# Performance work log

Hardware: AMD Instinct MI355X
Metric: run time of the kernel (lower is better)

Reference implementation:

```python
import jax, jax.numpy as jnp
import numpy as np


def _next_pow2(n: int) -> int:
    return 1 << (int(n) - 1).bit_length()


def setup_inputs() -> dict:
    key = jax.random.key(0)
    k1, k2 = jax.random.split(key)
    B, T, L = 256, 65536, 65536  # batch, seq_len, filter length (L >= T so epoched recurrence == full causal conv)
    x = jax.random.normal(k1, (B, T), dtype=jnp.float32)
    filt = jax.random.normal(k2, (1, L), dtype=jnp.float32) / np.float32(np.sqrt(L))
    return {"x": x, "filt": filt}


def reference(x, filt):
    """EpochedFutureFill.forward == causal FIR convolution of x with filt.

    The torch module's per-token loop (sliced dot-product + FFT-refreshed
    FutureFill cache every K steps) computes exactly
        y[:, t] = sum_{s=0}^{t} filt[0, s] * x[:, t - s]
    for t < T <= L. We express that directly as one FFT convolution,
    mirroring the module's own future_fill (pow-2 rfft/irfft) math.
    """
    B, T = x.shape
    L = filt.shape[-1]
    n_fft = _next_pow2(T + L - 1)
    xf = jnp.fft.rfft(x, n=n_fft)        # (B, n_fft//2+1) complex
    ff = jnp.fft.rfft(filt, n=n_fft)     # (1, n_fft//2+1) complex, broadcasts over batch
    y_full = jnp.fft.irfft(xf * ff, n=n_fft)
    return y_full[:, :T]                 # causal part: (B, T)
```

## Files before the change

### kernel.cpp

```cpp
#include <hip/hip_runtime.h>


#define N_FFT 131072
#define N1    512
#define N2    256
#define T_LEN 65536
#define CB    128
#define PI_F  3.14159265358979323846f
#define R2_F  0.70710678118654752f

typedef __attribute__((ext_vector_type(2))) __fp16 h2;
typedef __attribute__((ext_vector_type(4))) __fp16 h4;
typedef __attribute__((ext_vector_type(8))) __fp16 h8;

__device__ inline int brev9(int x) { return (int)(__brev((unsigned)x) >> 23); }

__device__ inline float2 cadd(float2 a, float2 b){ return make_float2(a.x+b.x, a.y+b.y); }
__device__ inline float2 csub(float2 a, float2 b){ return make_float2(a.x-b.x, a.y-b.y); }
__device__ inline float2 cmul(float2 a, float2 b){ return make_float2(a.x*b.x-a.y*b.y, a.x*b.y+a.y*b.x); }
__device__ inline float2 csq(float2 a){ return make_float2(a.x*a.x-a.y*a.y, 2.f*a.x*a.y); }
__device__ inline float2 conjf(float2 a){ return make_float2(a.x, -a.y); }
__device__ inline float2 expif(float a){ float s,c; __sincosf(a,&s,&c); return make_float2(c,s); }
__device__ inline h2 f2h(float2 v){ return __builtin_amdgcn_cvt_pkrtz(v.x, v.y); }
__device__ inline float2 mul_ipow(float2 a, int g){
    float2 b = (g & 1) ? make_float2(-a.y, a.x) : a;
    return (g & 2) ? make_float2(-b.x, -b.y) : b;
}

__device__ inline void dif4(float2&a0, float2&a1, float2&a2, float2&a3, float2 w1, float2 w2){
    float2 s02 = cadd(a0,a2), d02 = csub(a0,a2);
    float2 s13 = cadd(a1,a3), d13 = csub(a1,a3);
    float2 b2 = cmul(w1,d02);
    float2 t  = cmul(w1,d13);
    float2 b3 = make_float2(t.y, -t.x);
    a0 = cadd(s02,s13);
    a1 = cmul(w2, csub(s02,s13));
    a2 = cadd(b2,b3);
    a3 = cmul(w2, csub(b2,b3));
}

__device__ inline void dit4i(float2&a0, float2&a1, float2&a2, float2&a3, float2 w1, float2 w2){
    float2 t1 = cmul(w1,a1), t3 = cmul(w1,a3);
    float2 u0 = cadd(a0,t1), u1 = csub(a0,t1);
    float2 u2 = cadd(a2,t3), u3 = csub(a2,t3);
    float2 s2 = cmul(w2,u2), s3 = cmul(w2,u3);
    a0 = cadd(u0,s2); a2 = csub(u0,s2);
    a1 = make_float2(u1.x - s3.y, u1.y + s3.x);
    a3 = make_float2(u1.x + s3.y, u1.y - s3.x);
}

template<bool HALF>
__global__ __launch_bounds__(512, 4) void fwd_cols(
    const float* __restrict__ re_base, const float* __restrict__ im_base,
    long long row_stride, void* __restrict__ dstv)
{
    __shared__ float2 s[N1 * 16];
    const int tile = blockIdx.x, row = blockIdx.y, tid = threadIdx.x;
    const int n2base = tile * 16;
    const float* rp = re_base + (long long)row * row_stride;
    const float* ip = im_base ? (im_base + (long long)row * row_stride) : nullptr;

    {
        const int cp = tid & 7, n1g = tid >> 3;
#pragma unroll
        for (int i = 0; i < 4; i++) {
            int n1 = n1g + 64 * i;
            int g  = n1 * N2 + n2base + 2 * cp;
            float2 a = *(const float2*)(rp + g);
            float2 b = ip ? *(const float2*)(ip + g) : make_float2(0.f, 0.f);
            s[n1 * 16 + 2 * cp]     = make_float2(a.x, b.x);
            s[n1 * 16 + 2 * cp + 1] = make_float2(a.y, b.y);
        }
    }
    __syncthreads();

    const int c = tid & 15, r = tid >> 4;

    {
        float2 w1 = expif((float)r * (-PI_F / 256.f));
        const float2 stp = make_float2(0.92387953251f, -0.38268343236f);
#pragma unroll
        for (int qq = 0; qq < 4; qq++) {
            int j = r + 32 * qq;
            float2 w2 = csq(w1);
            float2 a0 = s[j * 16 + c], a1 = s[(j + 128) * 16 + c];
            float2 b2 = cmul(w1, a0);
            float2 t  = cmul(w1, a1);
            float2 b3 = make_float2(t.y, -t.x);
            s[j * 16 + c]         = cadd(a0, a1);
            s[(j + 128) * 16 + c] = cmul(w2, csub(a0, a1));
            s[(j + 256) * 16 + c] = cadd(b2, b3);
            s[(j + 384) * 16 + c] = cmul(w2, csub(b2, b3));
            w1 = cmul(w1, stp);
        }
    }
    __syncthreads();

    {
        float2 w1 = expif((float)r * (-PI_F / 64.f));
        float2 w2 = csq(w1);
#pragma unroll
        for (int qq = 0; qq < 4; qq++) {
            int p0 = qq * 128 + r;
            float2 a0 = s[p0*16+c], a1 = s[(p0+32)*16+c], a2 = s[(p0+64)*16+c], a3 = s[(p0+96)*16+c];
            dif4(a0, a1, a2, a3, w1, w2);
            s[p0*16+c] = a0; s[(p0+32)*16+c] = a1; s[(p0+64)*16+c] = a2; s[(p0+96)*16+c] = a3;
        }
    }
    __syncthreads();

    {
        float2 w1 = expif((float)(r & 7) * (-PI_F / 16.f));
        float2 w2 = csq(w1);
#pragma unroll
        for (int qq = 0; qq < 4; qq++) {
            int g = (r >> 3) + 4 * qq;
            int p0 = g * 32 + (r & 7);
            float2 a0 = s[p0*16+c], a1 = s[(p0+8)*16+c], a2 = s[(p0+16)*16+c], a3 = s[(p0+24)*16+c];
            dif4(a0, a1, a2, a3, w1, w2);
            s[p0*16+c] = a0; s[(p0+8)*16+c] = a1; s[(p0+16)*16+c] = a2; s[(p0+24)*16+c] = a3;
        }
    }
    __syncthreads();

    const int n2 = n2base + c;
    const float2 w1c = make_float2(R2_F, -R2_F);
    const float2 w2c = make_float2(0.f, -1.f);
    const float2 one = make_float2(1.f, 0.f);
    const float2 w64 = expif((float)n2 * (-PI_F / 1024.f));
#pragma unroll
    for (int o = 0; o < 2; o++) {
        int base = 8 * (r + 32 * o);
        float2 v[8];
#pragma unroll
        for (int m = 0; m < 8; m++) v[m] = s[(base + m) * 16 + c];
        dif4(v[0], v[2], v[4], v[6], one, one);
        dif4(v[1], v[3], v[5], v[7], w1c, w2c);
#pragma unroll
        for (int m = 0; m < 8; m += 2) {
            float2 a = v[m], b = v[m + 1];
            v[m] = cadd(a, b); v[m + 1] = csub(a, b);
        }
        const int Kb = brev9(base);
        float2 wK = expif((float)(n2 * Kb) * (-2.f * PI_F / (float)N_FFT));
        float2 pw[8];
        pw[0] = one;
#pragma unroll
        for (int k = 1; k < 8; k++) pw[k] = cmul(pw[k-1], w64);
        const int b3tab[8] = {0,4,2,6,1,5,3,7};
#pragma unroll
        for (int m = 0; m < 8; m++) {
            int b  = b3tab[m];
            int k1 = Kb + 64 * b;
            float2 w = cmul(wK, pw[b]);
            float2 rv = cmul(v[m], w);
            if (HALF) {
                h2* drow = (h2*)dstv + (size_t)row * N_FFT;
                drow[(size_t)k1 * N2 + n2] = f2h(rv);
            } else {
                float2* drow = (float2*)dstv + (size_t)row * N_FFT;
                drow[(size_t)k1 * N2 + n2] = rv;
            }
        }
    }
}

#define MROW 288
#define MIDX(rw, p) ((rw) * MROW + (p) + 2 * ((p) >> 4))

__global__ __launch_bounds__(256) void fwd_rows_g(float2* __restrict__ G)
{
    __shared__ float2 s[8 * MROW];
    const int tid = threadIdx.x;
    const long long rbase = (long long)blockIdx.x * 8;
#pragma unroll
    for (int i = 0; i < 8; i++) {
        int e = tid + 256 * i, rw = e >> 8, p = e & 255;
        s[MIDX(rw, p)] = G[(rbase + rw) * N2 + p];
    }
    __syncthreads();
    const int rl = tid >> 5, rr = tid & 31;
#pragma unroll
    for (int qq = 0; qq < 2; qq++) {
        int j = rr + 32 * qq;
        float2 w1 = expif((float)j * (-PI_F / 128.f)), w2 = csq(w1);
        float2 a0=s[MIDX(rl,j)], a1=s[MIDX(rl,j+64)], a2=s[MIDX(rl,j+128)], a3=s[MIDX(rl,j+192)];
        dif4(a0,a1,a2,a3,w1,w2);
        s[MIDX(rl,j)]=a0; s[MIDX(rl,j+64)]=a1; s[MIDX(rl,j+128)]=a2; s[MIDX(rl,j+192)]=a3;
    }
    __syncthreads();
#pragma unroll
    for (int qq = 0; qq < 2; qq++) {
        int q = rr + 32 * qq, j = q & 15, g = q >> 4, p0 = g * 64 + j;
        float2 w1 = expif((float)j * (-PI_F / 32.f)), w2 = csq(w1);
        float2 a0=s[MIDX(rl,p0)], a1=s[MIDX(rl,p0+16)], a2=s[MIDX(rl,p0+32)], a3=s[MIDX(rl,p0+48)];
        dif4(a0,a1,a2,a3,w1,w2);
        s[MIDX(rl,p0)]=a0; s[MIDX(rl,p0+16)]=a1; s[MIDX(rl,p0+32)]=a2; s[MIDX(rl,p0+48)]=a3;
    }
    __syncthreads();
#pragma unroll
    for (int qq = 0; qq < 2; qq++) {
        int q = rr + 32 * qq, j = q & 3, g = q >> 2, p0 = g * 16 + j;
        float2 w1 = expif((float)j * (-PI_F / 8.f)), w2 = csq(w1);
        float2 a0=s[MIDX(rl,p0)], a1=s[MIDX(rl,p0+4)], a2=s[MIDX(rl,p0+8)], a3=s[MIDX(rl,p0+12)];
        dif4(a0,a1,a2,a3,w1,w2);
        s[MIDX(rl,p0)]=a0; s[MIDX(rl,p0+4)]=a1; s[MIDX(rl,p0+8)]=a2; s[MIDX(rl,p0+12)]=a3;
    }
    __syncthreads();
#pragma unroll
    for (int qq = 0; qq < 2; qq++) {
        int base = 4 * (rr + 32 * qq);
        float2 a0=s[MIDX(rl,base)], a1=s[MIDX(rl,base+1)], a2=s[MIDX(rl,base+2)], a3=s[MIDX(rl,base+3)];
        float2 s02 = cadd(a0,a2), d02 = csub(a0,a2);
        float2 s13 = cadd(a1,a3), d13 = csub(a1,a3);
        float2 b3 = make_float2(d13.y, -d13.x);
        s[MIDX(rl,base)]   = cadd(s02,s13);
        s[MIDX(rl,base+1)] = csub(s02,s13);
        s[MIDX(rl,base+2)] = cadd(d02,b3);
        s[MIDX(rl,base+3)] = csub(d02,b3);
    }
    __syncthreads();
#pragma unroll
    for (int i = 0; i < 8; i++) {
        int e = tid + 256 * i, rw = e >> 8, p = e & 255;
        G[(rbase + rw) * N2 + p] = s[MIDX(rw, p)];
    }
}

__global__ __launch_bounds__(512) void mid_rows(
    h2* __restrict__ buf, const float2* __restrict__ Gb)
{
    __shared__ float4 s4[(8 * MROW) / 2];
    float2* s = (float2*)s4;
    const int tid = threadIdx.x;
    const long long rbase = (long long)blockIdx.x * 8;

    const int rl = tid >> 6, rr = tid & 63;
    const int k1 = (int)((rbase + rl) & (N1 - 1));

    const int rB = rl * MROW;
    const int b1 = rB + rr + ((rr >> 4) << 1);
    const int b2 = rB + 72 * (rr >> 4) + (rr & 15);
    const int b3 = rB + 18 * (rr >> 2) + (rr & 3);
    const int si = 144 * rl + 2 * rr + (rr >> 2);

    const float2 u0 = expif((float)rr * (-PI_F / 128.f));
    const float2 u1 = csq(csq(u0));
    const float2 u2 = csq(csq(u1));
    const float2 f2 = mul_ipow(u1, rr >> 4);
    const float2 f3 = mul_ipow(u2, rr >> 2);

    {
        h8 v = *((const h8*)(buf + ((rbase + rl) * N2 + 4 * rr)));
        s4[si]     = make_float4((float)v[0], (float)v[1], (float)v[2], (float)v[3]);
        s4[si + 1] = make_float4((float)v[4], (float)v[5], (float)v[6], (float)v[7]);
    }
    __syncthreads();

    {
        float2 w2 = csq(u0);
        float2 a0=s[b1], a1=s[b1+72], a2=s[b1+144], a3=s[b1+216];
        dif4(a0,a1,a2,a3,u0,w2);
        s[b1]=a0; s[b1+72]=a1; s[b1+144]=a2; s[b1+216]=a3;
    }
    __syncthreads();
    {
        float2 w2 = csq(f2);
        float2 a0=s[b2], a1=s[b2+18], a2=s[b2+36], a3=s[b2+54];
        dif4(a0,a1,a2,a3,f2,w2);
        s[b2]=a0; s[b2+18]=a1; s[b2+36]=a2; s[b2+54]=a3;
    }
    __syncthreads();
    {
        float2 w2 = csq(f3);
        float2 a0=s[b3], a1=s[b3+4], a2=s[b3+8], a3=s[b3+12];
        dif4(a0,a1,a2,a3,f3,w2);
        s[b3]=a0; s[b3+4]=a1; s[b3+8]=a2; s[b3+12]=a3;
    }
    __syncthreads();

    {
        int base = 4 * rr;
        float4 q01 = s4[si], q23 = s4[si + 1];
        float2 a0 = make_float2(q01.x, q01.y), a1 = make_float2(q01.z, q01.w);
        float2 a2 = make_float2(q23.x, q23.y), a3 = make_float2(q23.z, q23.w);
        float2 s02 = cadd(a0,a2), d02 = csub(a0,a2);
        float2 s13 = cadd(a1,a3), d13 = csub(a1,a3);
        float2 b3v = make_float2(d13.y, -d13.x);
        float2 v0 = cadd(s02,s13), v1 = csub(s02,s13), v2 = cadd(d02,b3v), v3 = csub(d02,b3v);
        const float4* g4 = (const float4*)(Gb + (size_t)k1 * N2);
        float4 g01 = g4[base >> 1], g23 = g4[(base >> 1) + 1];
        v0 = cmul(v0, make_float2(g01.x, g01.y));
        v1 = cmul(v1, make_float2(g01.z, g01.w));
        v2 = cmul(v2, make_float2(g23.x, g23.y));
        v3 = cmul(v3, make_float2(g23.z, g23.w));
        float2 u0v = cadd(v0,v1), u1v = csub(v0,v1);
        float2 u2v = cadd(v2,v3), u3v = csub(v2,v3);
        float2 r0 = cadd(u0v,u2v), r2 = csub(u0v,u2v);
        float2 r1 = make_float2(u1v.x - u3v.y, u1v.y + u3v.x);
        float2 r3 = make_float2(u1v.x + u3v.y, u1v.y - u3v.x);
        s4[si]     = make_float4(r0.x, r0.y, r1.x, r1.y);
        s4[si + 1] = make_float4(r2.x, r2.y, r3.x, r3.y);
    }
    __syncthreads();

    {
        float2 w2 = conjf(f3), w1 = csq(w2);
        float2 a0=s[b3], a1=s[b3+4], a2=s[b3+8], a3=s[b3+12];
        dit4i(a0,a1,a2,a3,w1,w2);
        s[b3]=a0; s[b3+4]=a1; s[b3+8]=a2; s[b3+12]=a3;
    }
    __syncthreads();
    {
        float2 w2 = conjf(f2), w1 = csq(w2);
        float2 a0=s[b2], a1=s[b2+18], a2=s[b2+36], a3=s[b2+54];
        dit4i(a0,a1,a2,a3,w1,w2);
        s[b2]=a0; s[b2+18]=a1; s[b2+36]=a2; s[b2+54]=a3;
    }
    __syncthreads();
    {
        float2 w2 = conjf(u0), w1 = csq(w2);
        float2 a0=s[b1], a1=s[b1+72], a2=s[b1+144], a3=s[b1+216];
        dit4i(a0,a1,a2,a3,w1,w2);
        s[b1]=a0; s[b1+72]=a1; s[b1+144]=a2; s[b1+216]=a3;
    }
    __syncthreads();

    {
        const int pp0 = 4 * rr;
        const float th = 2.f * PI_F / (float)N_FFT;
        float2 w = expif((float)(pp0 * k1) * th);
        float2 stp = expif((float)k1 * th);
        float4 q01 = s4[si], q23 = s4[si + 1];
        float2 r0 = cmul(make_float2(q01.x, q01.y), w); w = cmul(w, stp);
        float2 r1 = cmul(make_float2(q01.z, q01.w), w); w = cmul(w, stp);
        float2 r2 = cmul(make_float2(q23.x, q23.y), w); w = cmul(w, stp);
        float2 r3 = cmul(make_float2(q23.z, q23.w), w);
        union { h8 v8; h2 v2[4]; } U;
        U.v2[0] = f2h(r0); U.v2[1] = f2h(r1); U.v2[2] = f2h(r2); U.v2[3] = f2h(r3);
        *((h8*)(buf + ((rbase + rl) * N2 + pp0))) = U.v8;
    }
}

__global__ __launch_bounds__(512, 4) void inv_cols(
    const h2* __restrict__ src, float* __restrict__ out)
{
    __shared__ float4 s4[N1 * 16 / 2];
    float2* s = (float2*)s4;
    const int tile = blockIdx.x, row = blockIdx.y, tid = threadIdx.x;
    const int n2base = tile * 16;
    const h2* srow = src + (size_t)row * N_FFT;
    const int cp = tid & 7, r8 = tid >> 3;

#pragma unroll
    for (int i = 0; i < 8; i++) {
        int k1 = r8 + 64 * i;
        h4 v = *((const h4*)(srow + (size_t)k1 * N2 + n2base + 2 * cp));
        int p = brev9(k1);
        s4[p * 8 + cp] = make_float4((float)v.x, (float)v.y, (float)v.z, (float)v.w);
    }
    __syncthreads();

    const int c = tid & 15, r = tid >> 4;

    const float2 w1c = make_float2(0.f, 1.f);
    const float2 w2c = make_float2(R2_F, R2_F);
    const float2 one = make_float2(1.f, 0.f);
#pragma unroll
    for (int o = 0; o < 2; o++) {
        int base = 8 * (r + 32 * o);
        float2 v[8];
#pragma unroll
        for (int m = 0; m < 8; m++) v[m] = s[(base + m) * 16 + c];
#pragma unroll
        for (int m = 0; m < 8; m += 2) {
            float2 a = v[m], b = v[m + 1];
            v[m] = cadd(a, b); v[m + 1] = csub(a, b);
        }
        dit4i(v[0], v[2], v[4], v[6], one, one);
        dit4i(v[1], v[3], v[5], v[7], w1c, w2c);
#pragma unroll
        for (int m = 0; m < 8; m++) s[(base + m) * 16 + c] = v[m];
    }
    __syncthreads();

    {
        float2 w2 = expif((float)(r & 7) * (PI_F / 16.f));
        float2 w1 = csq(w2);
#pragma unroll
        for (int qq = 0; qq < 4; qq++) {
            int g = (r >> 3) + 4 * qq;
            int p0 = g * 32 + (r & 7);
            float2 a0 = s[p0*16+c], a1 = s[(p0+8)*16+c], a2 = s[(p0+16)*16+c], a3 = s[(p0+24)*16+c];
            dit4i(a0, a1, a2, a3, w1, w2);
            s[p0*16+c] = a0; s[(p0+8)*16+c] = a1; s[(p0+16)*16+c] = a2; s[(p0+24)*16+c] = a3;
        }
    }
    __syncthreads();
    {
        float2 w2 = expif((float)r * (PI_F / 64.f));
        float2 w1 = csq(w2);
#pragma unroll
        for (int qq = 0; qq < 4; qq++) {
            int p0 = qq * 128 + r;
            float2 a0 = s[p0*16+c], a1 = s[(p0+32)*16+c], a2 = s[(p0+64)*16+c], a3 = s[(p0+96)*16+c];
            dit4i(a0, a1, a2, a3, w1, w2);
            s[p0*16+c] = a0; s[(p0+32)*16+c] = a1; s[(p0+64)*16+c] = a2; s[(p0+96)*16+c] = a3;
        }
    }
    __syncthreads();
    {
        float2 w2 = expif((float)r * (PI_F / 256.f));
        const float2 stp = make_float2(0.92387953251f, 0.38268343236f);
#pragma unroll
        for (int qq = 0; qq < 4; qq++) {
            int j = r + 32 * qq;
            float2 w1 = csq(w2);
            float2 a0 = s[j*16+c], a1 = s[(j+128)*16+c], a2 = s[(j+256)*16+c], a3 = s[(j+384)*16+c];
            dit4i(a0, a1, a2, a3, w1, w2);
            s[j*16+c] = a0; s[(j+128)*16+c] = a1; s[(j+256)*16+c] = a2; s[(j+384)*16+c] = a3;
            w2 = cmul(w2, stp);
        }
    }
    __syncthreads();

    const float scale = 1.0f / (float)N_FFT;
    float* out0 = out + (size_t)(2 * row) * T_LEN;
    float* out1 = out + (size_t)(2 * row + 1) * T_LEN;
#pragma unroll
    for (int i = 0; i < 4; i++) {
        int p = r8 + 64 * i;
        float4 q = s4[p * 8 + cp];
        int n = p * N2 + n2base + 2 * cp;
        *(float2*)(out0 + n) = make_float2(q.x * scale, q.z * scale);
        *(float2*)(out1 + n) = make_float2(q.y * scale, q.w * scale);
    }
}

extern "C" void kernel_launch(void* const* d_in, const int* in_sizes, int n_in,
                              void* d_out, int out_size, void* d_ws, size_t ws_size,
                              hipStream_t stream) {
    const float* x    = (const float*)d_in[0];
    const float* filt = (const float*)d_in[1];
    float* out = (float*)d_out;

    h2* buf = (h2*)d_ws;
    float2* G = (float2*)((char*)d_ws + (size_t)CB * N_FFT * sizeof(h2));

    fwd_cols<false><<<dim3(16, 1), 512, 0, stream>>>(filt, nullptr, 0LL, (void*)G);
    fwd_rows_g<<<N1 / 8, 256, 0, stream>>>(G);
    fwd_cols<true><<<dim3(16, CB), 512, 0, stream>>>(x, x + T_LEN, (long long)(2 * T_LEN), (void*)buf);
    mid_rows<<<(CB * N1) / 8, 512, 0, stream>>>(buf, G);
    inv_cols<<<dim3(16, CB), 512, 0, stream>>>(buf, out);
}
```

Before: 232.4 us.

## Rewrite 256-point row FFTs as register-resident 16x16 decomposition

Replaces the radix-4 shared-memory passes in fwd_rows_g and mid_rows, which needed several barriers, with a 16x16 four-step FFT. Each thread holds 16 points in registers and does two fft16 passes with one LDS transpose, using a shared twiddle table. Each 16-lane row group syncs only with an lgkmcnt wait, and mid_rows now handles 16 rows per 256-thread block. This cuts LDS traffic, barriers and per-thread sincos work. The cost is more registers per thread and narrower h2 global loads and stores with a 16-element stride.

```diff
diff --git a/kernel.cpp b/kernel.cpp
--- a/kernel.cpp
+++ b/kernel.cpp
@@ -8,6 +8,8 @@
 #define CB    128
 #define PI_F  3.14159265358979323846f
 #define R2_F  0.70710678118654752f
+#define C16F  0.92387953251128675613f
+#define S16F  0.38268343236508977173f
 
 typedef __attribute__((ext_vector_type(2))) __fp16 h2;
 typedef __attribute__((ext_vector_type(4))) __fp16 h4;
@@ -18,14 +20,18 @@
 __device__ inline float2 cadd(float2 a, float2 b){ return make_float2(a.x+b.x, a.y+b.y); }
 __device__ inline float2 csub(float2 a, float2 b){ return make_float2(a.x-b.x, a.y-b.y); }
 __device__ inline float2 cmul(float2 a, float2 b){ return make_float2(a.x*b.x-a.y*b.y, a.x*b.y+a.y*b.x); }
+__device__ inline float2 cmulc(float2 a, float2 b){ return make_float2(a.x*b.x+a.y*b.y, a.y*b.x-a.x*b.y); }
 __device__ inline float2 csq(float2 a){ return make_float2(a.x*a.x-a.y*a.y, 2.f*a.x*a.y); }
 __device__ inline float2 conjf(float2 a){ return make_float2(a.x, -a.y); }
 __device__ inline float2 expif(float a){ float s,c; __sincosf(a,&s,&c); return make_float2(c,s); }
 __device__ inline h2 f2h(float2 v){ return __builtin_amdgcn_cvt_pkrtz(v.x, v.y); }
-__device__ inline float2 mul_ipow(float2 a, int g){
-    float2 b = (g & 1) ? make_float2(-a.y, a.x) : a;
-    return (g & 2) ? make_float2(-b.x, -b.y) : b;
-}
+
+__device__ inline float2 mul_mi(float2 a){ return make_float2(a.y, -a.x); }
+__device__ inline float2 mul_pi(float2 a){ return make_float2(-a.y, a.x); }
+__device__ inline float2 mul_w81(float2 a){ return make_float2(R2_F*(a.x+a.y), R2_F*(a.y-a.x)); }
+__device__ inline float2 mul_w83(float2 a){ return make_float2(R2_F*(a.y-a.x), -R2_F*(a.x+a.y)); }
+__device__ inline float2 mul_w81c(float2 a){ return make_float2(R2_F*(a.x-a.y), R2_F*(a.x+a.y)); }
+__device__ inline float2 mul_w83c(float2 a){ return make_float2(-R2_F*(a.x+a.y), R2_F*(a.x-a.y)); }
 
 __device__ inline void dif4(float2&a0, float2&a1, float2&a2, float2&a3, float2 w1, float2 w2){
     float2 s02 = cadd(a0,a2), d02 = csub(a0,a2);
@@ -47,6 +53,99 @@
     a0 = cadd(u0,s2); a2 = csub(u0,s2);
     a1 = make_float2(u1.x - s3.y, u1.y + s3.x);
     a3 = make_float2(u1.x + s3.y, u1.y - s3.x);
+}
+
+__device__ constexpr int BR[16] = {0,8,4,12,2,10,6,14,1,9,5,13,3,11,7,15};
+
+__device__ __forceinline__ void fft16_fwd(float2 v[16]){
+    {
+        float2 s02=cadd(v[0],v[8]),  d02=csub(v[0],v[8]);
+        float2 s13=cadd(v[4],v[12]), d13=csub(v[4],v[12]);
+        float2 b3 = mul_mi(d13);
+        v[0]=cadd(s02,s13); v[4]=csub(s02,s13);
+        v[8]=cadd(d02,b3);  v[12]=csub(d02,b3);
+    }
+    {
+        float2 s02=cadd(v[1],v[9]),  d02=csub(v[1],v[9]);
+        float2 s13=cadd(v[5],v[13]), d13=csub(v[5],v[13]);
+        const float2 w1 = make_float2(C16F,-S16F);
+        float2 b2 = cmul(w1,d02), b3 = mul_mi(cmul(w1,d13));
+        v[1]=cadd(s02,s13);  v[5]=mul_w81(csub(s02,s13));
+        v[9]=cadd(b2,b3);    v[13]=mul_w81(csub(b2,b3));
+    }
+    {
+        float2 s02=cadd(v[2],v[10]), d02=csub(v[2],v[10]);
+        float2 s13=cadd(v[6],v[14]), d13=csub(v[6],v[14]);
+        float2 b2 = mul_w81(d02), b3 = mul_mi(mul_w81(d13));
+        v[2]=cadd(s02,s13);  v[6]=mul_mi(csub(s02,s13));
+        v[10]=cadd(b2,b3);   v[14]=mul_mi(csub(b2,b3));
+    }
+    {
+        float2 s02=cadd(v[3],v[11]), d02=csub(v[3],v[11]);
+        float2 s13=cadd(v[7],v[15]), d13=csub(v[7],v[15]);
+        const float2 w1 = make_float2(S16F,-C16F);
+        float2 b2 = cmul(w1,d02), b3 = mul_mi(cmul(w1,d13));
+        v[3]=cadd(s02,s13);  v[7]=mul_w83(csub(s02,s13));
+        v[11]=cadd(b2,b3);   v[15]=mul_w83(csub(b2,b3));
+    }
+#pragma unroll
+    for (int q=0;q<4;q++){
+        float2 a0=v[4*q],a1=v[4*q+1],a2=v[4*q+2],a3=v[4*q+3];
+        float2 s02=cadd(a0,a2), d02=csub(a0,a2);
+        float2 s13=cadd(a1,a3), d13=csub(a1,a3);
+        float2 b3 = mul_mi(d13);
+        v[4*q]=cadd(s02,s13);   v[4*q+1]=csub(s02,s13);
+        v[4*q+2]=cadd(d02,b3);  v[4*q+3]=csub(d02,b3);
+    }
+}
+
+__device__ __forceinline__ void fft16_inv(float2 v[16]){
+#pragma unroll
+    for (int q=0;q<4;q++){
+        float2 a0=v[4*q],a1=v[4*q+1],a2=v[4*q+2],a3=v[4*q+3];
+        float2 u0=cadd(a0,a1), u1=csub(a0,a1);
+        float2 u2=cadd(a2,a3), u3=csub(a2,a3);
+        v[4*q]=cadd(u0,u2);   v[4*q+2]=csub(u0,u2);
+        v[4*q+1]=make_float2(u1.x-u3.y, u1.y+u3.x);
+        v[4*q+3]=make_float2(u1.x+u3.y, u1.y-u3.x);
+    }
+    {
+        float2 t1=v[4], t3=v[12];
+        float2 u0=cadd(v[0],t1), u1=csub(v[0],t1);
+        float2 u2=cadd(v[8],t3), u3=csub(v[8],t3);
+        v[0]=cadd(u0,u2); v[8]=csub(u0,u2);
+        v[4]=make_float2(u1.x-u3.y, u1.y+u3.x);
+        v[12]=make_float2(u1.x+u3.y, u1.y-u3.x);
+    }
+    {
+        float2 t1=mul_w81c(v[5]), t3=mul_w81c(v[13]);
+        float2 u0=cadd(v[1],t1), u1=csub(v[1],t1);
+        float2 u2=cadd(v[9],t3), u3=csub(v[9],t3);
+        const float2 w2 = make_float2(C16F,S16F);
+        float2 s2=cmul(w2,u2), s3=cmul(w2,u3);
+        v[1]=cadd(u0,s2); v[9]=csub(u0,s2);
+        v[5]=make_float2(u1.x-s3.y, u1.y+s3.x);
+        v[13]=make_float2(u1.x+s3.y, u1.y-s3.x);
+    }
+    {
+        float2 t1=mul_pi(v[6]), t3=mul_pi(v[14]);
+        float2 u0=cadd(v[2],t1), u1=csub(v[2],t1);
+        float2 u2=cadd(v[10],t3), u3=csub(v[10],t3);
+        float2 s2=mul_w81c(u2), s3=mul_w81c(u3);
+        v[2]=cadd(u0,s2); v[10]=csub(u0,s2);
+        v[6]=make_float2(u1.x-s3.y, u1.y+s3.x);
+        v[14]=make_float2(u1.x+s3.y, u1.y-s3.x);
+    }
+    {
+        float2 t1=mul_w83c(v[7]), t3=mul_w83c(v[15]);
+        float2 u0=cadd(v[3],t1), u1=csub(v[3],t1);
+        float2 u2=cadd(v[11],t3), u3=csub(v[11],t3);
+        const float2 w2 = make_float2(S16F,C16F);
+        float2 s2=cmul(w2,u2), s3=cmul(w2,u3);
+        v[3]=cadd(u0,s2); v[11]=csub(u0,s2);
+        v[7]=make_float2(u1.x-s3.y, u1.y+s3.x);
+        v[15]=make_float2(u1.x+s3.y, u1.y-s3.x);
+    }
 }
 
 template<bool HALF>
@@ -165,180 +264,128 @@
     }
 }
 
-#define MROW 288
-#define MIDX(rw, p) ((rw) * MROW + (p) + 2 * ((p) >> 4))
-
-__global__ __launch_bounds__(256) void fwd_rows_g(float2* __restrict__ G)
+#define RPITCH 18
+
+__global__ __launch_bounds__(128) void fwd_rows_g(float2* __restrict__ G)
 {
-    __shared__ float2 s[8 * MROW];
+    __shared__ __align__(16) float2 s[8 * 16 * RPITCH + 16 * RPITCH];
     const int tid = threadIdx.x;
-    const long long rbase = (long long)blockIdx.x * 8;
-#pragma unroll
-    for (int i = 0; i < 8; i++) {
-        int e = tid + 256 * i, rw = e >> 8, p = e & 255;
-        s[MIDX(rw, p)] = G[(rbase + rw) * N2 + p];
-    }
-    __syncthreads();
-    const int rl = tid >> 5, rr = tid & 31;
-#pragma unroll
-    for (int qq = 0; qq < 2; qq++) {
-        int j = rr + 32 * qq;
-        float2 w1 = expif((float)j * (-PI_F / 128.f)), w2 = csq(w1);
-        float2 a0=s[MIDX(rl,j)], a1=s[MIDX(rl,j+64)], a2=s[MIDX(rl,j+128)], a3=s[MIDX(rl,j+192)];
-        dif4(a0,a1,a2,a3,w1,w2);
-        s[MIDX(rl,j)]=a0; s[MIDX(rl,j+64)]=a1; s[MIDX(rl,j+128)]=a2; s[MIDX(rl,j+192)]=a3;
-    }
-    __syncthreads();
-#pragma unroll
-    for (int qq = 0; qq < 2; qq++) {
-        int q = rr + 32 * qq, j = q & 15, g = q >> 4, p0 = g * 64 + j;
-        float2 w1 = expif((float)j * (-PI_F / 32.f)), w2 = csq(w1);
-        float2 a0=s[MIDX(rl,p0)], a1=s[MIDX(rl,p0+16)], a2=s[MIDX(rl,p0+32)], a3=s[MIDX(rl,p0+48)];
-        dif4(a0,a1,a2,a3,w1,w2);
-        s[MIDX(rl,p0)]=a0; s[MIDX(rl,p0+16)]=a1; s[MIDX(rl,p0+32)]=a2; s[MIDX(rl,p0+48)]=a3;
-    }
-    __syncthreads();
-#pragma unroll
-    for (int qq = 0; qq < 2; qq++) {
-        int q = rr + 32 * qq, j = q & 3, g = q >> 2, p0 = g * 16 + j;
-        float2 w1 = expif((float)j * (-PI_F / 8.f)), w2 = csq(w1);
-        float2 a0=s[MIDX(rl,p0)], a1=s[MIDX(rl,p0+4)], a2=s[MIDX(rl,p0+8)], a3=s[MIDX(rl,p0+12)];
-        dif4(a0,a1,a2,a3,w1,w2);
-        s[MIDX(rl,p0)]=a0; s[MIDX(rl,p0+4)]=a1; s[MIDX(rl,p0+8)]=a2; s[MIDX(rl,p0+12)]=a3;
-    }
-    __syncthreads();
-#pragma unroll
-    for (int qq = 0; qq < 2; qq++) {
-        int base = 4 * (rr + 32 * qq);
-        float2 a0=s[MIDX(rl,base)], a1=s[MIDX(rl,base+1)], a2=s[MIDX(rl,base+2)], a3=s[MIDX(rl,base+3)];
-        float2 s02 = cadd(a0,a2), d02 = csub(a0,a2);
-        float2 s13 = cadd(a1,a3), d13 = csub(a1,a3);
-        float2 b3 = make_float2(d13.y, -d13.x);
-        s[MIDX(rl,base)]   = cadd(s02,s13);
-        s[MIDX(rl,base+1)] = csub(s02,s13);
-        s[MIDX(rl,base+2)] = cadd(d02,b3);
-        s[MIDX(rl,base+3)] = csub(d02,b3);
-    }
-    __syncthreads();
-#pragma unroll
-    for (int i = 0; i < 8; i++) {
-        int e = tid + 256 * i, rw = e >> 8, p = e & 255;
-        G[(rbase + rw) * N2 + p] = s[MIDX(rw, p)];
-    }
-}
-
-__global__ __launch_bounds__(512) void mid_rows(
-    h2* __restrict__ buf, const float2* __restrict__ Gb)
+    const int t = tid & 15, rl = tid >> 4;
+    const long long row = (long long)blockIdx.x * 8 + rl;
+    float2* tab = s + 8 * 16 * RPITCH;
+
+    {
+        int b0 = tid >> 4, c0 = tid & 15;
+        tab[b0 * RPITCH + c0] = expif((float)(b0 * c0) * (-2.f * PI_F / 256.f));
+        int e = tid + 128, b1 = e >> 4, c1 = e & 15;
+        tab[b1 * RPITCH + c1] = expif((float)(b1 * c1) * (-2.f * PI_F / 256.f));
+    }
+    __syncthreads();
+
+    const float2* gp = G + (size_t)row * N2 + t;
+    float2 v[16];
+#pragma unroll
+    for (int a = 0; a < 16; a++) v[a] = gp[16 * a];
+
+    fft16_fwd(v);
+#pragma unroll
+    for (int p = 1; p < 16; p++) v[p] = cmul(v[p], tab[t * RPITCH + BR[p]]);
+
+    float2* rS = s + rl * (16 * RPITCH);
+    float4* rS4 = (float4*)rS;
+#pragma unroll
+    for (int k = 0; k < 8; k++) {
+        float2 e = v[BR[2*k]], o = v[BR[2*k] + 8];
+        rS4[(t * RPITCH + 2*k) >> 1] = make_float4(e.x, e.y, o.x, o.y);
+    }
+    asm volatile("s_waitcnt lgkmcnt(0)" ::: "memory");
+#pragma unroll
+    for (int b = 0; b < 16; b++) v[b] = rS[b * RPITCH + t];
+
+    fft16_fwd(v);
+
+    float4* o4 = (float4*)(G + (size_t)row * N2 + 16 * t);
+#pragma unroll
+    for (int m = 0; m < 8; m++)
+        o4[m] = make_float4(v[2*m].x, v[2*m].y, v[2*m+1].x, v[2*m+1].y);
+}
+
+__global__ __launch_bounds__(256, 4) void mid_rows(
+    h2* __restrict__ buf, const float2* __restrict__ Gh)
 {
-    __shared__ float4 s4[(8 * MROW) / 2];
-    float2* s = (float2*)s4;
+    __shared__ __align__(16) float2 s[16 * 16 * RPITCH + 16 * RPITCH];
     const int tid = threadIdx.x;
-    const long long rbase = (long long)blockIdx.x * 8;
-
-    const int rl = tid >> 6, rr = tid & 63;
-    const int k1 = (int)((rbase + rl) & (N1 - 1));
-
-    const int rB = rl * MROW;
-    const int b1 = rB + rr + ((rr >> 4) << 1);
-    const int b2 = rB + 72 * (rr >> 4) + (rr & 15);
-    const int b3 = rB + 18 * (rr >> 2) + (rr & 3);
-    const int si = 144 * rl + 2 * rr + (rr >> 2);
-
-    const float2 u0 = expif((float)rr * (-PI_F / 128.f));
-    const float2 u1 = csq(csq(u0));
-    const float2 u2 = csq(csq(u1));
-    const float2 f2 = mul_ipow(u1, rr >> 4);
-    const float2 f3 = mul_ipow(u2, rr >> 2);
-
-    {
-        h8 v = *((const h8*)(buf + ((rbase + rl) * N2 + 4 * rr)));
-        s4[si]     = make_float4((float)v[0], (float)v[1], (float)v[2], (float)v[3]);
-        s4[si + 1] = make_float4((float)v[4], (float)v[5], (float)v[6], (float)v[7]);
-    }
-    __syncthreads();
-
-    {
-        float2 w2 = csq(u0);
-        float2 a0=s[b1], a1=s[b1+72], a2=s[b1+144], a3=s[b1+216];
-        dif4(a0,a1,a2,a3,u0,w2);
-        s[b1]=a0; s[b1+72]=a1; s[b1+144]=a2; s[b1+216]=a3;
-    }
-    __syncthreads();
-    {
-        float2 w2 = csq(f2);
-        float2 a0=s[b2], a1=s[b2+18], a2=s[b2+36], a3=s[b2+54];
-        dif4(a0,a1,a2,a3,f2,w2);
-        s[b2]=a0; s[b2+18]=a1; s[b2+36]=a2; s[b2+54]=a3;
-    }
-    __syncthreads();
-    {
-        float2 w2 = csq(f3);
-        float2 a0=s[b3], a1=s[b3+4], a2=s[b3+8], a3=s[b3+12];
-        dif4(a0,a1,a2,a3,f3,w2);
-        s[b3]=a0; s[b3+4]=a1; s[b3+8]=a2; s[b3+12]=a3;
-    }
-    __syncthreads();
-
-    {
-        int base = 4 * rr;
-        float4 q01 = s4[si], q23 = s4[si + 1];
-        float2 a0 = make_float2(q01.x, q01.y), a1 = make_float2(q01.z, q01.w);
-        float2 a2 = make_float2(q23.x, q23.y), a3 = make_float2(q23.z, q23.w);
-        float2 s02 = cadd(a0,a2), d02 = csub(a0,a2);
-        float2 s13 = cadd(a1,a3), d13 = csub(a1,a3);
-        float2 b3v = make_float2(d13.y, -d13.x);
-        float2 v0 = cadd(s02,s13), v1 = csub(s02,s13), v2 = cadd(d02,b3v), v3 = csub(d02,b3v);
-        const float4* g4 = (const float4*)(Gb + (size_t)k1 * N2);
-        float4 g01 = g4[base >> 1], g23 = g4[(base >> 1) + 1];
-        v0 = cmul(v0, make_float2(g01.x, g01.y));
-        v1 = cmul(v1, make_float2(g01.z, g01.w));
-        v2 = cmul(v2, make_float2(g23.x, g23.y));
-        v3 = cmul(v3, make_float2(g23.z, g23.w));
-        float2 u0v = cadd(v0,v1), u1v = csub(v0,v1);
-        float2 u2v = cadd(v2,v3), u3v = csub(v2,v3);
-        float2 r0 = cadd(u0v,u2v), r2 = csub(u0v,u2v);
-        float2 r1 = make_float2(u1v.x - u3v.y, u1v.y + u3v.x);
-        float2 r3 = make_float2(u1v.x + u3v.y, u1v.y - u3v.x);
-        s4[si]     = make_float4(r0.x, r0.y, r1.x, r1.y);
-        s4[si + 1] = make_float4(r2.x, r2.y, r3.x, r3.y);
-    }
-    __syncthreads();
-
-    {
-        float2 w2 = conjf(f3), w1 = csq(w2);
-        float2 a0=s[b3], a1=s[b3+4], a2=s[b3+8], a3=s[b3+12];
-        dit4i(a0,a1,a2,a3,w1,w2);
-        s[b3]=a0; s[b3+4]=a1; s[b3+8]=a2; s[b3+12]=a3;
-    }
-    __syncthreads();
-    {
-        float2 w2 = conjf(f2), w1 = csq(w2);
-        float2 a0=s[b2], a1=s[b2+18], a2=s[b2+36], a3=s[b2+54];
-        dit4i(a0,a1,a2,a3,w1,w2);
-        s[b2]=a0; s[b2+18]=a1; s[b2+36]=a2; s[b2+54]=a3;
-    }
-    __syncthreads();
-    {
-        float2 w2 = conjf(u0), w1 = csq(w2);
-        float2 a0=s[b1], a1=s[b1+72], a2=s[b1+144], a3=s[b1+216];
-        dit4i(a0,a1,a2,a3,w1,w2);
-        s[b1]=a0; s[b1+72]=a1; s[b1+144]=a2; s[b1+216]=a3;
-    }
-    __syncthreads();
-
-    {
-        const int pp0 = 4 * rr;
+    const int t = tid & 15, rl = tid >> 4;
+    const long long row = (long long)blockIdx.x * 16 + rl;
+    const int k1 = (int)(row & (N1 - 1));
+    float2* tab = s + 16 * 16 * RPITCH;
+
+    {
+        int b = tid >> 4, c = tid & 15;
+        tab[b * RPITCH + c] = expif((float)(b * c) * (-2.f * PI_F / 256.f));
+    }
+    __syncthreads();
+
+    h2* bp = buf + ((size_t)row * N2 + t);
+    float2 v[16];
+#pragma unroll
+    for (int a = 0; a < 16; a++) {
+        h2 h = bp[16 * a];
+        v[a] = make_float2((float)h.x, (float)h.y);
+    }
+
+    fft16_fwd(v);
+#pragma unroll
+    for (int p = 1; p < 16; p++) v[p] = cmul(v[p], tab[t * RPITCH + BR[p]]);
+
+    float2* rS = s + rl * (16 * RPITCH);
+    float4* rS4 = (float4*)rS;
+#pragma unroll
+    for (int k = 0; k < 8; k++) {
+        float2 e = v[BR[2*k]], o = v[BR[2*k] + 8];
+        rS4[(t * RPITCH + 2*k) >> 1] = make_float4(e.x, e.y, o.x, o.y);
+    }
+
+    const float4* g4 = (const float4*)(Gh + ((size_t)k1 * N2 + 16 * t));
+    float4 g[8];
+#pragma unroll
+    for (int m = 0; m < 8; m++) g[m] = g4[m];
+
+    asm volatile("s_waitcnt lgkmcnt(0)" ::: "memory");
+#pragma unroll
+    for (int b = 0; b < 16; b++) v[b] = rS[b * RPITCH + t];
+
+    fft16_fwd(v);
+
+#pragma unroll
+    for (int m = 0; m < 8; m++) {
+        v[2*m]   = cmul(v[2*m],   make_float2(g[m].x, g[m].y));
+        v[2*m+1] = cmul(v[2*m+1], make_float2(g[m].z, g[m].w));
+    }
+
+    fft16_inv(v);
+#pragma unroll
+    for (int b = 1; b < 16; b++) v[b] = cmulc(v[b], tab[b * RPITCH + t]);
+
+#pragma unroll
+    for (int m = 0; m < 8; m++)
+        rS4[(t * RPITCH + 2*m) >> 1] = make_float4(v[2*m].x, v[2*m].y, v[2*m+1].x, v[2*m+1].y);
+    asm volatile("s_waitcnt lgkmcnt(0)" ::: "memory");
+#pragma unroll
+    for (int c = 0; c < 16; c++) v[BR[c]] = rS[c * RPITCH + t];
+
+    fft16_inv(v);
+
+    {
         const float th = 2.f * PI_F / (float)N_FFT;
-        float2 w = expif((float)(pp0 * k1) * th);
-        float2 stp = expif((float)k1 * th);
-        float4 q01 = s4[si], q23 = s4[si + 1];
-        float2 r0 = cmul(make_float2(q01.x, q01.y), w); w = cmul(w, stp);
-        float2 r1 = cmul(make_float2(q01.z, q01.w), w); w = cmul(w, stp);
-        float2 r2 = cmul(make_float2(q23.x, q23.y), w); w = cmul(w, stp);
-        float2 r3 = cmul(make_float2(q23.z, q23.w), w);
-        union { h8 v8; h2 v2[4]; } U;
-        U.v2[0] = f2h(r0); U.v2[1] = f2h(r1); U.v2[2] = f2h(r2); U.v2[3] = f2h(r3);
-        *((h8*)(buf + ((rbase + rl) * N2 + pp0))) = U.v8;
+        float2 w = expif((float)(k1 * t) * th);
+        const float2 stp = expif((float)(16 * k1) * th);
+#pragma unroll
+        for (int a = 0; a < 16; a++) {
+            float2 r = cmul(v[a], w);
+            bp[16 * a] = f2h(r);
+            if (a < 15) w = cmul(w, stp);
+        }
     }
 }
 
@@ -448,8 +495,8 @@
     float2* G = (float2*)((char*)d_ws + (size_t)CB * N_FFT * sizeof(h2));
 
     fwd_cols<false><<<dim3(16, 1), 512, 0, stream>>>(filt, nullptr, 0LL, (void*)G);
-    fwd_rows_g<<<N1 / 8, 256, 0, stream>>>(G);
+    fwd_rows_g<<<N1 / 8, 128, 0, stream>>>(G);
     fwd_cols<true><<<dim3(16, CB), 512, 0, stream>>>(x, x + T_LEN, (long long)(2 * T_LEN), (void*)buf);
-    mid_rows<<<(CB * N1) / 8, 512, 0, stream>>>(buf, G);
+    mid_rows<<<(CB * N1) / 16, 256, 0, stream>>>(buf, G);
     inv_cols<<<dim3(16, CB), 512, 0, stream>>>(buf, out);
 }
```

Measured after the change: 220.4 us. 1.05x faster.
